# Kernel optimization log

Hardware: AMD Instinct MI355X
Metric: run time of the kernel (lower is better)

Reference implementation:

```python
import jax, jax.numpy as jnp
import numpy as np

N_NODES = 100000
N_EDGES = 1600000
D_FEAT = 128
HIDDEN = 64


def setup_inputs() -> dict:
    key = jax.random.key(0)
    k1, k2, k3, k4, k5 = jax.random.split(key, 5)
    x = jax.random.normal(k1, (N_NODES, D_FEAT), dtype=jnp.float32)
    edge_index = jax.random.randint(k2, (2, N_EDGES), 0, N_NODES, dtype=jnp.int32)
    edge_weight = jax.random.uniform(k3, (N_EDGES,), dtype=jnp.float32)
    W1 = jax.random.normal(k4, (D_FEAT, HIDDEN), dtype=jnp.float32) / np.sqrt(D_FEAT)
    b1 = jnp.zeros((HIDDEN,), dtype=jnp.float32)
    W2 = jax.random.normal(k5, (HIDDEN, 1), dtype=jnp.float32) / np.sqrt(HIDDEN)
    b2 = jnp.zeros((1,), dtype=jnp.float32)
    return {"x": x, "edge_index": edge_index, "edge_weight": edge_weight,
            "W1": W1, "b1": b1, "W2": W2, "b2": b2}


def reference(x, edge_index, edge_weight, W1, b1, W2, b2):
    N = x.shape[0]
    # PyG GCNConv default: add self-loops with weight 1.0
    loops = jnp.arange(N, dtype=edge_index.dtype)
    row = jnp.concatenate([edge_index[0], loops])  # source nodes
    col = jnp.concatenate([edge_index[1], loops])  # target nodes
    ew = jnp.concatenate([edge_weight, jnp.ones((N,), dtype=edge_weight.dtype)])
    # symmetric degree normalization: norm_e = d^{-1/2}[row] * w_e * d^{-1/2}[col]
    deg = jax.ops.segment_sum(ew, col, num_segments=N)
    dinv = jnp.where(deg > 0, jax.lax.rsqrt(deg), 0.0)
    norm = dinv[row] * ew * dinv[col]  # [E+N]

    def gcn_layer(h, W, b):
        h = h @ W                          # [N, out] transform first (PyG order)
        msg = h[row] * norm[:, None]       # gather + scale, [E+N, out]
        agg = jax.ops.segment_sum(msg, col, num_segments=N)  # scatter-add
        return agg + b

    h = jax.nn.relu(gcn_layer(x, W1, b1))
    # dropout(p=0.5) is identity in eval mode
    return gcn_layer(h, W2, b2)  # [N, 1]
```

## Files before the change

### kernel.cpp

```cpp
#include <hip/hip_runtime.h>
#include <stdint.h>

typedef float f4 __attribute__((ext_vector_type(4)));
typedef float f32x4 __attribute__((ext_vector_type(4)));
typedef _Float16 hq4 __attribute__((ext_vector_type(4)));
typedef _Float16 half8 __attribute__((ext_vector_type(8)));

#define DF 128
#define HID 64
#define EPB 4096
#define CAP 5120

__global__ __launch_bounds__(256) void kPrep(const float* __restrict__ W1,
                                             _Float16* __restrict__ W1f,
                                             int* __restrict__ cur, int nbin) {
    int t = blockIdx.x * 256 + threadIdx.x;
    if (t < nbin) cur[t] = 0;
    if (t < 8192) {
        int j     = t & 7;
        int lane  = (t >> 3) & 63;
        int ntile = (t >> 9) & 3;
        int kstep = t >> 11;
        int k = kstep * 32 + (lane >> 4) * 8 + j;
        int n = ntile * 16 + (lane & 15);
        W1f[t] = (_Float16)W1[k * 64 + n];
    }
}

__global__ __launch_bounds__(512) void kA3(const int* __restrict__ row,
                                           const int* __restrict__ col,
                                           const float* __restrict__ ew,
                                           int* __restrict__ cur,
                                           int2* __restrict__ tmp,
                                           int E, int nbin) {
    __shared__ int hist[512];
    __shared__ int pref[512];
    __shared__ int lbase[512];
    __shared__ int wsum[8];
    __shared__ int2 sv[EPB];
    __shared__ int  sa[EPB];
    int b = blockIdx.x, t = threadIdx.x;
    hist[t] = 0;
    __syncthreads();
    int s = b * EPB, e = min(E, s + EPB);
    int cnt = e - s;
    int  mybin[8], myrank[8];
    int2 myv[8];
#pragma unroll
    for (int k = 0; k < 8; ++k) {
        int i = s + t + k * 512;
        mybin[k] = -1;
        if (i < e) {
            int c = col[i];
            int bin = c >> 8;
            myv[k].x = row[i] | ((c & 255) << 24);
            myv[k].y = __float_as_int(ew[i]);
            mybin[k] = bin;
            myrank[k] = atomicAdd(&hist[bin], 1);
        }
    }
    __syncthreads();
    int val = hist[t];
    lbase[t] = val ? atomicAdd(&cur[t], val) + t * CAP : 0;
    int lane = t & 63, wid = t >> 6;
    int inc = val;
#pragma unroll
    for (int d = 1; d < 64; d <<= 1) {
        int y = __shfl_up(inc, d);
        if (lane >= d) inc += y;
    }
    if (lane == 63) wsum[wid] = inc;
    __syncthreads();
    if (t == 0) {
        int r = 0;
#pragma unroll
        for (int i = 0; i < 8; ++i) { int x = wsum[i]; wsum[i] = r; r += x; }
    }
    __syncthreads();
    pref[t] = inc - val + wsum[wid];
    __syncthreads();
#pragma unroll
    for (int k = 0; k < 8; ++k) {
        if (mybin[k] >= 0) {
            int pos = pref[mybin[k]] + myrank[k];
            sv[pos] = myv[k];
            sa[pos] = lbase[mybin[k]] + myrank[k];
        }
    }
    __syncthreads();
    for (int i = t; i < cnt; i += 512) tmp[sa[i]] = sv[i];
}

__global__ __launch_bounds__(512) void kB(const int2* __restrict__ tmp,
                                          const int* __restrict__ cur,
                                          int2* __restrict__ edata,
                                          int2* __restrict__ offse,
                                          float* __restrict__ dinv,
                                          int N) {
    __shared__ int   hist[256];
    __shared__ float degl[256];
    __shared__ int   fill[256];
    __shared__ int   wsum[8];
    __shared__ int2  se[CAP];
    int bin = blockIdx.x, t = threadIdx.x;
    int s = bin * CAP;
    int cnt = min(cur[bin], CAP);

    if (t < 256) { hist[t] = 0; degl[t] = 0.f; }
    __syncthreads();
    for (int i = t; i < cnt; i += 512) {
        int2 pr = tmp[s + i];
        se[i] = pr;
        int lo = ((unsigned)pr.x) >> 24;
        atomicAdd(&hist[lo], 1);
        atomicAdd(&degl[lo], __int_as_float(pr.y));
    }
    __syncthreads();
    int val = (t < 256) ? hist[t] : 0;
    int lane = t & 63, wid = t >> 6;
    int inc = val;
#pragma unroll
    for (int d = 1; d < 64; d <<= 1) {
        int y = __shfl_up(inc, d);
        if (lane >= d) inc += y;
    }
    if (lane == 63) wsum[wid] = inc;
    __syncthreads();
    if (t == 0) {
        int r = 0;
#pragma unroll
        for (int i = 0; i < 8; ++i) { int x = wsum[i]; wsum[i] = r; r += x; }
    }
    __syncthreads();
    int pfx = inc - val + wsum[wid];
    if (t < 256) {
        fill[t] = pfx;
        int c = bin * 256 + t;
        if (c < N) {
            int2 oe;
            oe.x = s + pfx;
            oe.y = s + pfx + val;
            offse[c] = oe;
            dinv[c] = rsqrtf(1.0f + degl[t]);
        }
    }
    __syncthreads();
    for (int i = t; i < cnt; i += 512) {
        int2 pr = se[i];
        int lo = ((unsigned)pr.x) >> 24;
        int pos = atomicAdd(&fill[lo], 1);
        int2 o;
        o.x = pr.x & 0x00FFFFFF;
        o.y = pr.y;
        edata[s + pos] = o;
    }
}

__global__ __launch_bounds__(256) void k_gemm1(const float* __restrict__ x,
                                               const _Float16* __restrict__ W1f,
                                               const float* __restrict__ dinv,
                                               _Float16* __restrict__ h, int N) {
    int wave  = (blockIdx.x * 256 + threadIdx.x) >> 6;
    int nstrip = (N + 15) >> 4;
    if (wave >= nstrip) return;
    int node0 = wave << 4;
    int l = threadIdx.x & 63;
    int quad = l >> 4;
    int m = l & 15;
    int r = node0 + m;
    if (r >= N) r = N - 1;

    const half8* bfrag = (const half8*)W1f;
    f32x4 acc[4];
#pragma unroll
    for (int nt = 0; nt < 4; ++nt) acc[nt] = (f32x4)(0.f);

#pragma unroll
    for (int kstep = 0; kstep < 4; ++kstep) {
        const f4* xr = (const f4*)(x + (size_t)r * DF + kstep * 32 + quad * 8);
        f4 a0 = xr[0], a1 = xr[1];
        half8 af;
        af[0] = (_Float16)a0.x; af[1] = (_Float16)a0.y;
        af[2] = (_Float16)a0.z; af[3] = (_Float16)a0.w;
        af[4] = (_Float16)a1.x; af[5] = (_Float16)a1.y;
        af[6] = (_Float16)a1.z; af[7] = (_Float16)a1.w;
#pragma unroll
        for (int nt = 0; nt < 4; ++nt) {
            half8 bf = bfrag[(kstep * 4 + nt) * 64 + l];
            acc[nt] = __builtin_amdgcn_mfma_f32_16x16x32_f16(af, bf, acc[nt], 0, 0, 0);
        }
    }

    float dv[4];
    int nodeb = node0 + quad * 4;
#pragma unroll
    for (int reg = 0; reg < 4; ++reg)
        dv[reg] = (nodeb + reg < N) ? dinv[nodeb + reg] : 0.f;
#pragma unroll
    for (int nt = 0; nt < 4; ++nt) {
#pragma unroll
        for (int reg = 0; reg < 4; ++reg) {
            int node = nodeb + reg;
            if (node < N)
                h[(unsigned)node * 64u + (unsigned)(nt * 16 + m)] =
                    (_Float16)(dv[reg] * acc[nt][reg]);
        }
    }
}

__global__ __launch_bounds__(256) void k_agg_h2(const int2* __restrict__ offse,
                                                const int2* __restrict__ edata,
                                                const float* __restrict__ dinv,
                                                const _Float16* __restrict__ h,
                                                const float* __restrict__ b1,
                                                const float* __restrict__ W2,
                                                float* __restrict__ h2p, int N) {
    __shared__ int2 stage[4][68];
    int wv = threadIdx.x >> 6;
    int l  = threadIdx.x & 63;
    int g  = l >> 4;
    unsigned fq = (unsigned)(l & 15);
    int sbase = g * 17;
    int vv = blockIdx.x * 16 + wv * 4 + g;
    bool ok = vv < N;
    int v = ok ? vv : N - 1;
    const hq4* hp = (const hq4*)h;

    float di = dinv[v];
    int2 oe = offse[v];

    hq4 sv4 = hp[((unsigned)v << 4) | fq];
    float a0 = (float)sv4.x, a1 = (float)sv4.y;
    float a2 = (float)sv4.z, a3 = (float)sv4.w;

    int deg = oe.y - oe.x;
    for (int base = 0; base < deg; base += 16) {
        int idx = oe.x + base + (int)fq;
        int2 pr;
        pr.x = 0; pr.y = 0;
        if (idx < oe.y) pr = edata[idx];
        stage[wv][sbase + (int)fq] = pr;
#pragma unroll
        for (int k = 0; k < 16; ++k) {
            int2 em = stage[wv][sbase + k];
            float w = __int_as_float(em.y);
            hq4 hv = hp[((unsigned)em.x << 4) | fq];
            a0 += w * (float)hv.x;
            a1 += w * (float)hv.y;
            a2 += w * (float)hv.z;
            a3 += w * (float)hv.w;
        }
    }

    a0 = di * a0; a1 = di * a1; a2 = di * a2; a3 = di * a3;
    f4 bb = ((const f4*)b1)[fq];
    f4 ww = ((const f4*)W2)[fq];
    float s = fmaxf(a0 + bb.x, 0.f) * ww.x
            + fmaxf(a1 + bb.y, 0.f) * ww.y
            + fmaxf(a2 + bb.z, 0.f) * ww.z
            + fmaxf(a3 + bb.w, 0.f) * ww.w;
    s += __shfl_down(s, 8);
    s += __shfl_down(s, 4);
    s += __shfl_down(s, 2);
    s += __shfl_down(s, 1);
    if (fq == 0 && ok) h2p[vv] = di * s;
}

__global__ __launch_bounds__(256) void k_out(const int2* __restrict__ offse,
                                             const int2* __restrict__ edata,
                                             const float* __restrict__ dinv,
                                             const float* __restrict__ h2p,
                                             const float* __restrict__ b2,
                                             float* __restrict__ out, int N) {
    int t = blockIdx.x * 256 + threadIdx.x;
    int v = t >> 4;
    if (v >= N) return;
    int c = t & 15;
    int2 oe = offse[v];
    float s = 0.f;
    for (int i = oe.x + c; i < oe.y; i += 16) {
        int2 pr = edata[i];
        s += __int_as_float(pr.y) * h2p[(unsigned)pr.x];
    }
    s += __shfl_down(s, 8);
    s += __shfl_down(s, 4);
    s += __shfl_down(s, 2);
    s += __shfl_down(s, 1);
    if (c == 0) {
        float di = dinv[v];
        out[v] = b2[0] + di * (h2p[v] + s);
    }
}

extern "C" void kernel_launch(void* const* d_in, const int* in_sizes, int n_in,
                              void* d_out, int out_size, void* d_ws, size_t ws_size,
                              hipStream_t stream) {
    const float* x  = (const float*)d_in[0];
    const int*   ei = (const int*)d_in[1];
    const float* ew = (const float*)d_in[2];
    const float* W1 = (const float*)d_in[3];
    const float* b1 = (const float*)d_in[4];
    const float* W2 = (const float*)d_in[5];
    const float* b2 = (const float*)d_in[6];
    float* out = (float*)d_out;

    const int N = in_sizes[0] / DF;
    const int E = in_sizes[2];
    const int* row = ei;
    const int* col = ei + E;

    const int nbin = (N + 255) / 256;
    const int nblk = (E + EPB - 1) / EPB;

    size_t    gsz   = (size_t)nbin * CAP;
    int*      w32   = (int*)d_ws;
    int2*     edata = (int2*)w32;
    int*      shreg = w32 + (size_t)2 * gsz;
    int2*     tmp   = (int2*)shreg;
    _Float16* h     = (_Float16*)shreg;
    int*      p     = shreg + (size_t)2 * gsz;
    int*      cur   = p;  p += ((nbin) + 3) & ~3;
    float*    dinv  = (float*)p;  p += N;
    float*    h2p   = (float*)p;  p += N;
    int2*     offse = (int2*)p;   p += 2 * N;
    _Float16* W1f   = (_Float16*)p;

    const int B = 256;
    int nstrip = (N + 15) / 16;
    int gGm  = (nstrip + 3) / 4;
    int gAgg = (N + 15) / 16;
    int gN16 = (N * 16 + B - 1) / B;

    kPrep<<<32, B, 0, stream>>>(W1, W1f, cur, nbin);
    kA3<<<nblk, 512, 0, stream>>>(row, col, ew, cur, tmp, E, nbin);
    kB<<<nbin, 512, 0, stream>>>(tmp, cur, edata, offse, dinv, N);
    k_gemm1<<<gGm, B, 0, stream>>>(x, W1f, dinv, h, N);
    k_agg_h2<<<gAgg, B, 0, stream>>>(offse, edata, dinv, h, b1, W2, h2p, N);
    k_out<<<gN16, B, 0, stream>>>(offse, edata, dinv, h2p, b2, out, N);
}
```

Baseline: 195.3 us.

## Co-schedule edge binning with X·W1 GEMM and fold dinv scaling into CSR build

Merges the edge-binning kernel and the dense X·W1 MFMA GEMM into one heterogeneous launch: the first blocks bin edges and the rest compute unscaled fp32 products into a new buffer g, each with its own fp16 W1 fragment copy in LDS. The per-bin CSR kernel then applies dinv and writes the fp16 h buffer, removing the separate GEMM kernel and the prep kernel (cur is now zeroed by a memset). The goal is to overlap the bandwidth-bound GEMM with the atomic-heavy binning and cut launches. In exchange it adds an extra fp32 N×64 write and read round trip through g, recomputes the W1 conversion in every GEMM block, and the fused kernel's large LDS footprint lowers occupancy for the GEMM blocks.

Result: slower. 204.3 us (+4.6%).

```diff
diff --git a/kernel.cpp b/kernel.cpp
--- a/kernel.cpp
+++ b/kernel.cpp
@@ -11,95 +11,140 @@
 #define EPB 4096
 #define CAP 5120
 
-__global__ __launch_bounds__(256) void kPrep(const float* __restrict__ W1,
-                                             _Float16* __restrict__ W1f,
-                                             int* __restrict__ cur, int nbin) {
-    int t = blockIdx.x * 256 + threadIdx.x;
-    if (t < nbin) cur[t] = 0;
-    if (t < 8192) {
-        int j     = t & 7;
-        int lane  = (t >> 3) & 63;
-        int ntile = (t >> 9) & 3;
-        int kstep = t >> 11;
-        int k = kstep * 32 + (lane >> 4) * 8 + j;
-        int n = ntile * 16 + (lane & 15);
-        W1f[t] = (_Float16)W1[k * 64 + n];
-    }
-}
-
-__global__ __launch_bounds__(512) void kA3(const int* __restrict__ row,
-                                           const int* __restrict__ col,
-                                           const float* __restrict__ ew,
-                                           int* __restrict__ cur,
-                                           int2* __restrict__ tmp,
-                                           int E, int nbin) {
-    __shared__ int hist[512];
-    __shared__ int pref[512];
-    __shared__ int lbase[512];
-    __shared__ int wsum[8];
-    __shared__ int2 sv[EPB];
-    __shared__ int  sa[EPB];
-    int b = blockIdx.x, t = threadIdx.x;
-    hist[t] = 0;
-    __syncthreads();
-    int s = b * EPB, e = min(E, s + EPB);
-    int cnt = e - s;
-    int  mybin[8], myrank[8];
-    int2 myv[8];
-#pragma unroll
-    for (int k = 0; k < 8; ++k) {
-        int i = s + t + k * 512;
-        mybin[k] = -1;
-        if (i < e) {
-            int c = col[i];
-            int bin = c >> 8;
-            myv[k].x = row[i] | ((c & 255) << 24);
-            myv[k].y = __float_as_int(ew[i]);
-            mybin[k] = bin;
-            myrank[k] = atomicAdd(&hist[bin], 1);
-        }
-    }
-    __syncthreads();
-    int val = hist[t];
-    lbase[t] = val ? atomicAdd(&cur[t], val) + t * CAP : 0;
-    int lane = t & 63, wid = t >> 6;
-    int inc = val;
-#pragma unroll
-    for (int d = 1; d < 64; d <<= 1) {
-        int y = __shfl_up(inc, d);
-        if (lane >= d) inc += y;
-    }
-    if (lane == 63) wsum[wid] = inc;
-    __syncthreads();
-    if (t == 0) {
-        int r = 0;
-#pragma unroll
-        for (int i = 0; i < 8; ++i) { int x = wsum[i]; wsum[i] = r; r += x; }
-    }
-    __syncthreads();
-    pref[t] = inc - val + wsum[wid];
-    __syncthreads();
-#pragma unroll
-    for (int k = 0; k < 8; ++k) {
-        if (mybin[k] >= 0) {
-            int pos = pref[mybin[k]] + myrank[k];
-            sv[pos] = myv[k];
-            sa[pos] = lbase[mybin[k]] + myrank[k];
-        }
-    }
-    __syncthreads();
-    for (int i = t; i < cnt; i += 512) tmp[sa[i]] = sv[i];
+__global__ __launch_bounds__(512) void kFused(const int* __restrict__ row,
+                                              const int* __restrict__ col,
+                                              const float* __restrict__ ew,
+                                              int* __restrict__ cur,
+                                              int2* __restrict__ tmp,
+                                              const float* __restrict__ x,
+                                              const float* __restrict__ W1,
+                                              float* __restrict__ g,
+                                              int E, int nblk, int nstrip, int N) {
+    __shared__ __align__(16) char smem[55360];
+    int t = threadIdx.x;
+
+    if ((int)blockIdx.x < nblk) {
+        int*  hist  = (int*)smem;
+        int*  pref  = hist + 512;
+        int*  lbase = pref + 512;
+        int*  wsum  = lbase + 512;
+        int2* sv    = (int2*)(smem + 6208);
+        int*  sa    = (int*)(smem + 6208 + 32768);
+        int b = blockIdx.x;
+        hist[t] = 0;
+        __syncthreads();
+        int s = b * EPB, e = min(E, s + EPB);
+        int cnt = e - s;
+        int  mybin[8], myrank[8];
+        int2 myv[8];
+#pragma unroll
+        for (int k = 0; k < 8; ++k) {
+            int i = s + t + k * 512;
+            mybin[k] = -1;
+            if (i < e) {
+                int c = col[i];
+                int bin = c >> 8;
+                myv[k].x = row[i] | ((c & 255) << 24);
+                myv[k].y = __float_as_int(ew[i]);
+                mybin[k] = bin;
+                myrank[k] = atomicAdd(&hist[bin], 1);
+            }
+        }
+        __syncthreads();
+        int val = hist[t];
+        lbase[t] = val ? atomicAdd(&cur[t], val) + t * CAP : 0;
+        int lane = t & 63, wid = t >> 6;
+        int inc = val;
+#pragma unroll
+        for (int d = 1; d < 64; d <<= 1) {
+            int y = __shfl_up(inc, d);
+            if (lane >= d) inc += y;
+        }
+        if (lane == 63) wsum[wid] = inc;
+        __syncthreads();
+        if (t == 0) {
+            int r = 0;
+#pragma unroll
+            for (int i = 0; i < 8; ++i) { int xx = wsum[i]; wsum[i] = r; r += xx; }
+        }
+        __syncthreads();
+        pref[t] = inc - val + wsum[wid];
+        __syncthreads();
+#pragma unroll
+        for (int k = 0; k < 8; ++k) {
+            if (mybin[k] >= 0) {
+                int pos = pref[mybin[k]] + myrank[k];
+                sv[pos] = myv[k];
+                sa[pos] = lbase[mybin[k]] + myrank[k];
+            }
+        }
+        __syncthreads();
+        for (int i = t; i < cnt; i += 512) tmp[sa[i]] = sv[i];
+    } else {
+        _Float16* W1f = (_Float16*)smem;
+        for (int i = t; i < 8192; i += 512) {
+            int j     = i & 7;
+            int lane  = (i >> 3) & 63;
+            int ntile = (i >> 9) & 3;
+            int kstep = i >> 11;
+            int k = kstep * 32 + (lane >> 4) * 8 + j;
+            int n = ntile * 16 + (lane & 15);
+            W1f[i] = (_Float16)W1[k * 64 + n];
+        }
+        __syncthreads();
+        int wave = ((int)blockIdx.x - nblk) * 8 + (t >> 6);
+        if (wave >= nstrip) return;
+        int node0 = wave << 4;
+        int l = t & 63;
+        int quad = l >> 4;
+        int m = l & 15;
+        int r = node0 + m;
+        if (r >= N) r = N - 1;
+
+        const half8* bfrag = (const half8*)W1f;
+        f32x4 acc[4];
+#pragma unroll
+        for (int nt = 0; nt < 4; ++nt) acc[nt] = (f32x4)(0.f);
+#pragma unroll
+        for (int kstep = 0; kstep < 4; ++kstep) {
+            const f4* xr = (const f4*)(x + (size_t)r * DF + kstep * 32 + quad * 8);
+            f4 a0 = xr[0], a1 = xr[1];
+            half8 af;
+            af[0] = (_Float16)a0.x; af[1] = (_Float16)a0.y;
+            af[2] = (_Float16)a0.z; af[3] = (_Float16)a0.w;
+            af[4] = (_Float16)a1.x; af[5] = (_Float16)a1.y;
+            af[6] = (_Float16)a1.z; af[7] = (_Float16)a1.w;
+#pragma unroll
+            for (int nt = 0; nt < 4; ++nt) {
+                half8 bf = bfrag[(kstep * 4 + nt) * 64 + l];
+                acc[nt] = __builtin_amdgcn_mfma_f32_16x16x32_f16(af, bf, acc[nt], 0, 0, 0);
+            }
+        }
+        int nodeb = node0 + quad * 4;
+#pragma unroll
+        for (int nt = 0; nt < 4; ++nt) {
+#pragma unroll
+            for (int reg = 0; reg < 4; ++reg) {
+                int node = nodeb + reg;
+                if (node < N)
+                    g[(size_t)node * 64 + (unsigned)(nt * 16 + m)] = acc[nt][reg];
+            }
+        }
+    }
 }
 
 __global__ __launch_bounds__(512) void kB(const int2* __restrict__ tmp,
                                           const int* __restrict__ cur,
+                                          const float* __restrict__ g,
                                           int2* __restrict__ edata,
                                           int2* __restrict__ offse,
                                           float* __restrict__ dinv,
+                                          _Float16* __restrict__ h,
                                           int N) {
     __shared__ int   hist[256];
     __shared__ float degl[256];
     __shared__ int   fill[256];
+    __shared__ float dl[256];
     __shared__ int   wsum[8];
     __shared__ int2  se[CAP];
     int bin = blockIdx.x, t = threadIdx.x;
@@ -136,13 +181,16 @@
     if (t < 256) {
         fill[t] = pfx;
         int c = bin * 256 + t;
+        float di = 0.f;
         if (c < N) {
             int2 oe;
             oe.x = s + pfx;
             oe.y = s + pfx + val;
             offse[c] = oe;
-            dinv[c] = rsqrtf(1.0f + degl[t]);
-        }
+            di = rsqrtf(1.0f + degl[t]);
+            dinv[c] = di;
+        }
+        dl[t] = di;
     }
     __syncthreads();
     for (int i = t; i < cnt; i += 512) {
@@ -154,57 +202,13 @@
         o.y = pr.y;
         edata[s + pos] = o;
     }
-}
-
-__global__ __launch_bounds__(256) void k_gemm1(const float* __restrict__ x,
-                                               const _Float16* __restrict__ W1f,
-                                               const float* __restrict__ dinv,
-                                               _Float16* __restrict__ h, int N) {
-    int wave  = (blockIdx.x * 256 + threadIdx.x) >> 6;
-    int nstrip = (N + 15) >> 4;
-    if (wave >= nstrip) return;
-    int node0 = wave << 4;
-    int l = threadIdx.x & 63;
-    int quad = l >> 4;
-    int m = l & 15;
-    int r = node0 + m;
-    if (r >= N) r = N - 1;
-
-    const half8* bfrag = (const half8*)W1f;
-    f32x4 acc[4];
-#pragma unroll
-    for (int nt = 0; nt < 4; ++nt) acc[nt] = (f32x4)(0.f);
-
-#pragma unroll
-    for (int kstep = 0; kstep < 4; ++kstep) {
-        const f4* xr = (const f4*)(x + (size_t)r * DF + kstep * 32 + quad * 8);
-        f4 a0 = xr[0], a1 = xr[1];
-        half8 af;
-        af[0] = (_Float16)a0.x; af[1] = (_Float16)a0.y;
-        af[2] = (_Float16)a0.z; af[3] = (_Float16)a0.w;
-        af[4] = (_Float16)a1.x; af[5] = (_Float16)a1.y;
-        af[6] = (_Float16)a1.z; af[7] = (_Float16)a1.w;
-#pragma unroll
-        for (int nt = 0; nt < 4; ++nt) {
-            half8 bf = bfrag[(kstep * 4 + nt) * 64 + l];
-            acc[nt] = __builtin_amdgcn_mfma_f32_16x16x32_f16(af, bf, acc[nt], 0, 0, 0);
-        }
-    }
-
-    float dv[4];
-    int nodeb = node0 + quad * 4;
-#pragma unroll
-    for (int reg = 0; reg < 4; ++reg)
-        dv[reg] = (nodeb + reg < N) ? dinv[nodeb + reg] : 0.f;
-#pragma unroll
-    for (int nt = 0; nt < 4; ++nt) {
-#pragma unroll
-        for (int reg = 0; reg < 4; ++reg) {
-            int node = nodeb + reg;
-            if (node < N)
-                h[(unsigned)node * 64u + (unsigned)(nt * 16 + m)] =
-                    (_Float16)(dv[reg] * acc[nt][reg]);
-        }
+    int vbase = bin << 8;
+    for (int i = t; i < 256 * 64; i += 512) {
+        int c = i >> 6;
+        int v = vbase + c;
+        if (v < N)
+            h[(size_t)v * 64 + (i & 63)] =
+                (_Float16)(dl[c] * g[(size_t)v * 64 + (i & 63)]);
     }
 }
 
@@ -313,28 +317,25 @@
     const int nblk = (E + EPB - 1) / EPB;
 
     size_t    gsz   = (size_t)nbin * CAP;
-    int*      w32   = (int*)d_ws;
-    int2*     edata = (int2*)w32;
-    int*      shreg = w32 + (size_t)2 * gsz;
-    int2*     tmp   = (int2*)shreg;
-    _Float16* h     = (_Float16*)shreg;
-    int*      p     = shreg + (size_t)2 * gsz;
-    int*      cur   = p;  p += ((nbin) + 3) & ~3;
-    float*    dinv  = (float*)p;  p += N;
-    float*    h2p   = (float*)p;  p += N;
-    int2*     offse = (int2*)p;   p += 2 * N;
-    _Float16* W1f   = (_Float16*)p;
+    int2*     edata = (int2*)d_ws;
+    int2*     tmp   = edata + gsz;
+    float*    g     = (float*)(tmp + gsz);
+    _Float16* h     = (_Float16*)(g + (size_t)N * 64);
+    float*    dinv  = (float*)(h + (size_t)N * 64);
+    float*    h2p   = dinv + N;
+    int2*     offse = (int2*)(h2p + N);
+    int*      cur   = (int*)(offse + N);
 
     const int B = 256;
     int nstrip = (N + 15) / 16;
-    int gGm  = (nstrip + 3) / 4;
+    int gemmBlocks = (nstrip + 7) / 8;
     int gAgg = (N + 15) / 16;
     int gN16 = (N * 16 + B - 1) / B;
 
-    kPrep<<<32, B, 0, stream>>>(W1, W1f, cur, nbin);
-    kA3<<<nblk, 512, 0, stream>>>(row, col, ew, cur, tmp, E, nbin);
-    kB<<<nbin, 512, 0, stream>>>(tmp, cur, edata, offse, dinv, N);
-    k_gemm1<<<gGm, B, 0, stream>>>(x, W1f, dinv, h, N);
+    hipMemsetAsync(cur, 0, nbin * sizeof(int), stream);
+    kFused<<<nblk + gemmBlocks, 512, 0, stream>>>(row, col, ew, cur, tmp,
+                                                  x, W1, g, E, nblk, nstrip, N);
+    kB<<<nbin, 512, 0, stream>>>(tmp, cur, g, edata, offse, dinv, h, N);
     k_agg_h2<<<gAgg, B, 0, stream>>>(offse, edata, dinv, h, b1, W2, h2p, N);
     k_out<<<gN16, B, 0, stream>>>(offse, edata, dinv, h2p, b2, out, N);
 }
```
